# Kernel tuning notes

Hardware: AMD Instinct MI355X
Metric: run time of the kernel (lower is better)

## Reference

```python
import jax, jax.numpy as jnp
import numpy as np

C = 256      # in/out channels
PSI = 4
W = C // PSI          # window width = 64
D = W // 2            # stride = 32
HEADS = 2 * PSI - 1   # 7


def conv_bn_relu(x, Wmat, scale, bias):
    # 1x1 conv (no bias) + inference-mode BN (folded to per-channel scale/bias) + ReLU
    y = jnp.einsum('oc,bcn->bon', Wmat, x)
    return jax.nn.relu(y * scale[:, None] + bias[:, None])


def setup_inputs() -> dict:
    key = jax.random.key(0)
    ks = jax.random.split(key, 16)
    B, N = 4, 2048
    x = jax.random.normal(ks[0], (B, C, N), dtype=jnp.float32)
    Wq = jax.random.normal(ks[1], (C, C), dtype=jnp.float32) / np.sqrt(C)
    Wk = jax.random.normal(ks[2], (C, C), dtype=jnp.float32) / np.sqrt(C)
    Wv = jax.random.normal(ks[3], (C, C), dtype=jnp.float32) / np.sqrt(C)
    sq = jax.random.uniform(ks[4], (C,), dtype=jnp.float32, minval=0.5, maxval=1.5)
    bq = jax.random.normal(ks[5], (C,), dtype=jnp.float32) * 0.1
    sk = jax.random.uniform(ks[6], (C,), dtype=jnp.float32, minval=0.5, maxval=1.5)
    bk = jax.random.normal(ks[7], (C,), dtype=jnp.float32) * 0.1
    sv = jax.random.uniform(ks[8], (C,), dtype=jnp.float32, minval=0.5, maxval=1.5)
    bv = jax.random.normal(ks[9], (C,), dtype=jnp.float32) * 0.1
    Wf = jax.random.normal(ks[10], (C, HEADS * W), dtype=jnp.float32) / np.sqrt(HEADS * W)
    bf = jax.random.normal(ks[11], (C,), dtype=jnp.float32) * 0.1
    sf = jax.random.uniform(ks[12], (C,), dtype=jnp.float32, minval=0.5, maxval=1.5)
    bff = jax.random.normal(ks[13], (C,), dtype=jnp.float32) * 0.1
    return dict(x=x, Wq=Wq, sq=sq, bq=bq, Wk=Wk, sk=sk, bk=bk,
                Wv=Wv, sv=sv, bv=bv, Wf=Wf, bf=bf, sf=sf, bff=bff)


def reference(x, Wq, sq, bq, Wk, sk, bk, Wv, sv, bv, Wf, bf, sf, bff):
    q = conv_bn_relu(x, Wq, sq, bq)   # [B, C, N]
    k = conv_bn_relu(x, Wk, sk, bk)
    v = conv_bn_relu(x, Wv, sv, bv)

    # overlapping channel windows: head m covers channels [m*D, m*D+W)
    win = jnp.arange(HEADS)[:, None] * D + jnp.arange(W)[None, :]  # [HEADS, W]
    qw = q[:, win, :]  # [B, HEADS, W, N]
    kw = k[:, win, :]
    vw = v[:, win, :]

    # a_m = q_m^T k_m over channel window -> [B, HEADS, N, N]
    attn = jnp.einsum('bhwn,bhwm->bhnm', qw, kw)
    attn = jax.nn.softmax(attn, axis=-1)
    # o_m = (a_m v_m^T)^T -> [B, HEADS, W, N]
    o = jnp.einsum('bhnm,bhwm->bhwn', attn, vw)

    B, _, _, N = o.shape
    O = o.reshape(B, HEADS * W, N)  # concat heads along channel dim

    # fusion: 1x1 conv (with bias) + BN + ReLU
    y = jnp.einsum('oc,bcn->bon', Wf, O) + bf[:, None]
    return jax.nn.relu(y * sf[:, None] + bff[:, None])
```

## Files before the change

### kernel.cpp

```cpp
#include <hip/hip_runtime.h>
#include <hip/hip_bf16.h>

typedef __attribute__((ext_vector_type(8))) short bf16x8;
typedef __attribute__((ext_vector_type(4))) float f32x4;

namespace {
constexpr int kC = 256;
constexpr int kN = 2048;
constexpr int kB = 4;
constexpr int kHeads = 7;
constexpr int kOC = kHeads * 64;
constexpr int kSplit = 2;
constexpr int kMChunk = kN / kSplit;
constexpr float kLog2e = 1.44269504f;
}

static __device__ __forceinline__ float bf2f(ushort u) {
    union { unsigned u; float f; } v; v.u = ((unsigned)u) << 16;
    return v.f;
}
static __device__ __forceinline__ unsigned pk_bf16(float a, float b) {
    __hip_bfloat162 h = __float22bfloat162_rn(make_float2(a, b));
    union { __hip_bfloat162 h; unsigned u; } v; v.h = h;
    return v.u;
}
static __device__ __forceinline__ ushort4 pack4bf(float a, float b, float c, float d) {
    union { ushort4 s; uint2 u; } v;
    v.u.x = pk_bf16(a, b); v.u.y = pk_bf16(c, d);
    return v.s;
}
static __device__ __forceinline__ float fexp2(float x) {
#if __has_builtin(__builtin_amdgcn_exp2f)
    return __builtin_amdgcn_exp2f(x);
#else
    return exp2f(x);
#endif
}
static __device__ __forceinline__ void g2l16(const ushort* g, ushort* l) {
    __builtin_amdgcn_global_load_lds(
        (const __attribute__((address_space(1))) void*)g,
        (__attribute__((address_space(3))) void*)l,
        16, 0, 0);
}

__global__ __launch_bounds__(256) void cast_w_kernel(
    const float* __restrict__ Wq, const float* __restrict__ Wk,
    const float* __restrict__ Wv, const float* __restrict__ Wf,
    ushort* __restrict__ wq, ushort* __restrict__ wk,
    ushort* __restrict__ wv, ushort* __restrict__ wf)
{
    int which = blockIdx.y;
    const float* src = which == 0 ? Wq : which == 1 ? Wk : which == 2 ? Wv : Wf;
    ushort* dst      = which == 0 ? wq : which == 1 ? wk : which == 2 ? wv : wf;
    int n = (which == 3) ? kC * kOC : kC * kC;
    int i = (blockIdx.x * 256 + threadIdx.x) * 4;
    if (i < n) {
        float4 v = *(const float4*)(src + i);
        *(ushort4*)(dst + i) = pack4bf(v.x, v.y, v.z, v.w);
    }
}

__global__ __launch_bounds__(256) void transpose_kernel(
    const float* __restrict__ x, ushort* __restrict__ xT)
{
    const int nt = blockIdx.x, ct = blockIdx.y, b = blockIdx.z;
    __shared__ float T[64][65];
    const int tid = threadIdx.x;
    const float* xb = x + ((size_t)b * kC + ct * 64) * kN + nt * 64;
#pragma unroll
    for (int p = 0; p < 16; ++p) {
        int idx = p * 256 + tid;
        int cc = idx >> 6, nn = idx & 63;
        T[cc][nn] = xb[(size_t)cc * kN + nn];
    }
    __syncthreads();
    ushort* xTb = xT + ((size_t)b * kN + nt * 64) * kC + ct * 64;
#pragma unroll
    for (int p = 0; p < 4; ++p) {
        int nn = p * 16 + (tid >> 4);
        int c4 = (tid & 15) * 4;
        *(ushort4*)&xTb[(size_t)nn * kC + c4] =
            pack4bf(T[c4 + 0][nn], T[c4 + 1][nn], T[c4 + 2][nn], T[c4 + 3][nn]);
    }
}

__global__ __launch_bounds__(256, 2) void qkv_kernel(
    const ushort* __restrict__ xT,
    const ushort* __restrict__ Wqb, const ushort* __restrict__ Wkb, const ushort* __restrict__ Wvb,
    const float* __restrict__ sq, const float* __restrict__ bq,
    const float* __restrict__ sk, const float* __restrict__ bk,
    const float* __restrict__ sv, const float* __restrict__ bv,
    ushort* __restrict__ qT, ushort* __restrict__ kT, ushort* __restrict__ vB)
{
    const int nt  = blockIdx.x;
    const int ot  = blockIdx.y;
    const int b   = blockIdx.z / 3;
    const int mat = blockIdx.z % 3;
    const ushort* Wb = mat == 0 ? Wqb : mat == 1 ? Wkb : Wvb;
    const float* sm = mat == 0 ? sq : mat == 1 ? sk : sv;
    const float* bm = mat == 0 ? bq : mat == 1 ? bk : bv;

    __shared__ __align__(16) ushort lds[4][128 * 64];

    const int tid = threadIdx.x;
    const int lane = tid & 63, wav = tid >> 6;
    const int quad = lane >> 4, l16 = lane & 15;

    const ushort* xTb = xT + ((size_t)b * kN + nt * 128) * kC;
    const ushort* Wt  = Wb + (size_t)(ot * 128) * kC;

    f32x4 acc[8][2];
#pragma unroll
    for (int mt = 0; mt < 8; ++mt)
#pragma unroll
        for (int ntt = 0; ntt < 2; ++ntt)
#pragma unroll
            for (int r = 0; r < 4; ++r) acc[mt][ntt][r] = 0.f;

    const int sa   = lane >> 3;
    const int sblk = (lane & 7) ^ sa;
    auto dmaK = [&](int k0, int buf) {
#pragma unroll
        for (int p = 0; p < 4; ++p) {
            int row = wav * 32 + p * 8 + sa;
            size_t so = (size_t)row * kC + k0 + sblk * 8;
            int dbase = (wav * 32 + p * 8) * 64;
            g2l16(Wt + so,  &lds[buf][dbase]);
            g2l16(xTb + so, &lds[2 + buf][dbase]);
        }
    };

    dmaK(0, 0);
    __syncthreads();

    for (int kt = 0; kt < 4; ++kt) {
        const int cur = kt & 1;
        const bool more = (kt < 3);
        if (more) dmaK((kt + 1) * 64, cur ^ 1);

        const ushort* rowB = (mat < 2) ? lds[cur] : lds[2 + cur];
        const ushort* colB = (mat < 2) ? lds[2 + cur] : lds[cur];
#pragma unroll
        for (int ks = 0; ks < 2; ++ks) {
            bf16x8 bfr[2];
#pragma unroll
            for (int ntt = 0; ntt < 2; ++ntt) {
                int row = wav * 32 + ntt * 16 + l16;
                bfr[ntt] = *(const bf16x8*)&colB[row * 64 + (((ks * 4 + quad) ^ (row & 7)) * 8)];
            }
#pragma unroll
            for (int mt = 0; mt < 8; ++mt) {
                int row = mt * 16 + l16;
                bf16x8 af = *(const bf16x8*)&rowB[row * 64 + (((ks * 4 + quad) ^ (row & 7)) * 8)];
#pragma unroll
                for (int ntt = 0; ntt < 2; ++ntt)
                    acc[mt][ntt] = __builtin_amdgcn_mfma_f32_16x16x32_bf16(
                        af, bfr[ntt], acc[mt][ntt], 0, 0, 0);
            }
        }
        __syncthreads();
    }

    ushort* sT = &lds[0][0];
    const float qs = (mat == 0) ? kLog2e : 1.f;

    if (mat < 2) {
#pragma unroll
        for (int mt = 0; mt < 8; ++mt) {
            float4 sc4 = *(const float4*)&sm[ot * 128 + mt * 16 + quad * 4];
            float4 bi4 = *(const float4*)&bm[ot * 128 + mt * 16 + quad * 4];
#pragma unroll
            for (int ntt = 0; ntt < 2; ++ntt) {
                int nrow = wav * 32 + ntt * 16 + l16;
                float v0 = fmaf(acc[mt][ntt][0], sc4.x, bi4.x) * qs;
                float v1 = fmaf(acc[mt][ntt][1], sc4.y, bi4.y) * qs;
                float v2 = fmaf(acc[mt][ntt][2], sc4.z, bi4.z) * qs;
                float v3 = fmaf(acc[mt][ntt][3], sc4.w, bi4.w) * qs;
                int cb = (mt * 2 + (quad >> 1)) ^ (nrow & 15);
                *(ushort4*)&sT[nrow * 128 + cb * 8 + (quad & 1) * 4] =
                    pack4bf(v0 > 0.f ? v0 : 0.f, v1 > 0.f ? v1 : 0.f,
                            v2 > 0.f ? v2 : 0.f, v3 > 0.f ? v3 : 0.f);
            }
        }
        __syncthreads();
        ushort* out = (mat == 0) ? qT : kT;
#pragma unroll
        for (int p = 0; p < 8; ++p) {
            int idx = p * 256 + tid;
            int row = idx >> 4, blk = idx & 15;
            int4 d = *(const int4*)&sT[row * 128 + ((blk ^ (row & 15)) * 8)];
            *(int4*)&out[((size_t)b * kN + nt * 128 + row) * kC + ot * 128 + blk * 8] = d;
        }
    } else {
#pragma unroll
        for (int ntt = 0; ntt < 2; ++ntt) {
            int orow = wav * 32 + ntt * 16 + l16;
            float sc = sm[ot * 128 + orow], bi = bm[ot * 128 + orow];
#pragma unroll
            for (int mt = 0; mt < 8; ++mt) {
                float v0 = fmaf(acc[mt][ntt][0], sc, bi);
                float v1 = fmaf(acc[mt][ntt][1], sc, bi);
                float v2 = fmaf(acc[mt][ntt][2], sc, bi);
                float v3 = fmaf(acc[mt][ntt][3], sc, bi);
                int cb = (mt * 2 + (quad >> 1)) ^ (orow & 15);
                *(ushort4*)&sT[orow * 128 + cb * 8 + (quad & 1) * 4] =
                    pack4bf(v0 > 0.f ? v0 : 0.f, v1 > 0.f ? v1 : 0.f,
                            v2 > 0.f ? v2 : 0.f, v3 > 0.f ? v3 : 0.f);
            }
        }
        __syncthreads();
#pragma unroll
        for (int p = 0; p < 8; ++p) {
            int idx = p * 256 + tid;
            int row = idx >> 4, blk = idx & 15;
            int4 d = *(const int4*)&sT[row * 128 + ((blk ^ (row & 15)) * 8)];
            *(int4*)&vB[((size_t)b * kC + ot * 128 + row) * kN + nt * 128 + blk * 8] = d;
        }
    }
}

__global__ __launch_bounds__(512, 4) void attn_kernel(
    const ushort* __restrict__ qT, const ushort* __restrict__ kT,
    const ushort* __restrict__ vB,
    ushort* __restrict__ Opart, float* __restrict__ Ls)
{
    const int j   = blockIdx.x;
    const int lid = (j & 7) * 56 + (j >> 3);
    const int nt  = lid & 7;
    const int rest = lid >> 3;
    const int h = rest % 7;
    const int z = rest / 7;
    const int s = z & 1;
    const int b = z >> 1;
    const int n0 = nt * 256;

    const int tid = threadIdx.x;
    const int lane = tid & 63, wav = tid >> 6;
    const int quad = lane >> 4, l16 = lane & 15;

    __shared__ __align__(16) ushort sKV[2][8192];

    const ushort* qTb = qT + (size_t)b * kN * kC;
    const ushort* kTb = kT + (size_t)b * kN * kC;
    const ushort* vbb = vB + ((size_t)b * kC + h * 32) * kN;

    const int arr   = wav >> 2;
    const int rbase = (wav & 3) * 16;

    bf16x8 qf[2][2];
#pragma unroll
    for (int kk = 0; kk < 2; ++kk)
#pragma unroll
        for (int nt2 = 0; nt2 < 2; ++nt2) {
            int ng = n0 + wav * 32 + nt2 * 16 + l16;
            qf[kk][nt2] = *(const bf16x8*)(qTb + (size_t)ng * kC + h * 32 + kk * 32 + quad * 8);
        }

    f32x4 oacc[4][2];
#pragma unroll
    for (int wt = 0; wt < 4; ++wt)
#pragma unroll
        for (int nt2 = 0; nt2 < 2; ++nt2)
#pragma unroll
            for (int r = 0; r < 4; ++r) oacc[wt][nt2][r] = 0.f;
    float li[2] = {0.f, 0.f};

    const int mstart = s * kMChunk;
    const int NIT = kMChunk / 64;

    const int sa   = lane >> 3;
    const int sblk = (lane & 7) ^ sa;
    auto dmaTile = [&](int m0, int buf) {
#pragma unroll
        for (int p = 0; p < 2; ++p) {
            int rl = rbase + p * 8 + sa;
            const ushort* src = (arr == 0)
                ? (kTb + (size_t)(m0 + rl) * kC + h * 32 + sblk * 8)
                : (vbb + (size_t)rl * kN + m0 + sblk * 8);
            g2l16(src, &sKV[buf][arr * 4096 + (rbase + p * 8) * 64]);
        }
    };

    dmaTile(mstart, 0);
    __syncthreads();

    for (int it = 0; it < NIT; ++it) {
        const int cur = it & 1;
        const bool more = (it + 1 < NIT);
        if (more) dmaTile(mstart + (it + 1) * 64, cur ^ 1);

        const ushort* sK = &sKV[cur][0];
        const ushort* sV = &sKV[cur][4096];

        f32x4 sacc[4][2];
#pragma unroll
        for (int mt = 0; mt < 4; ++mt)
#pragma unroll
            for (int nt2 = 0; nt2 < 2; ++nt2)
#pragma unroll
                for (int r = 0; r < 4; ++r) sacc[mt][nt2][r] = 0.f;
        __builtin_amdgcn_s_setprio(1);
#pragma unroll
        for (int kk = 0; kk < 2; ++kk)
#pragma unroll
            for (int mt = 0; mt < 4; ++mt) {
                int row = mt * 16 + l16;
                bf16x8 af = *(const bf16x8*)&sK[row * 64 + (((kk * 4 + quad) ^ (row & 7)) * 8)];
#pragma unroll
                for (int nt2 = 0; nt2 < 2; ++nt2)
                    sacc[mt][nt2] = __builtin_amdgcn_mfma_f32_16x16x32_bf16(
                        af, qf[kk][nt2], sacc[mt][nt2], 0, 0, 0);
            }
        __builtin_amdgcn_s_setprio(0);

        unsigned d[2][4][2];
#pragma unroll
        for (int nt2 = 0; nt2 < 2; ++nt2) {
            float sum = 0.f;
#pragma unroll
            for (int mt = 0; mt < 4; ++mt) {
                float p0 = fexp2(sacc[mt][nt2][0]);
                float p1 = fexp2(sacc[mt][nt2][1]);
                float p2 = fexp2(sacc[mt][nt2][2]);
                float p3 = fexp2(sacc[mt][nt2][3]);
                sum += (p0 + p1) + (p2 + p3);
                d[nt2][mt][0] = pk_bf16(p0, p1);
                d[nt2][mt][1] = pk_bf16(p2, p3);
            }
            sum += __shfl_xor(sum, 16);
            sum += __shfl_xor(sum, 32);
            li[nt2] += sum;
        }

#pragma unroll
        for (int ks = 0; ks < 2; ++ks) {
            bf16x8 pf[2];
#pragma unroll
            for (int nt2 = 0; nt2 < 2; ++nt2) {
                union { unsigned w[4]; bf16x8 v8; } pu;
#if __has_builtin(__builtin_amdgcn_permlane32_swap) && __has_builtin(__builtin_amdgcn_permlane16_swap)
#pragma unroll
                for (int rd = 0; rd < 2; ++rd) {
                    unsigned a = d[nt2][2 * ks][rd], bb = d[nt2][2 * ks + 1][rd];
                    auto r32 = __builtin_amdgcn_permlane32_swap(a, bb, false, false);
                    auto r16 = __builtin_amdgcn_permlane16_swap(r32[0], r32[1], false, false);
                    pu.w[rd]     = r16[0];
                    pu.w[2 + rd] = r16[1];
                }
#else
                const int gx = ((lane & 16) << 1) + l16;
                const int gy = gx + 16;
                const bool lo = (lane < 32);
#pragma unroll
                for (int rd = 0; rd < 2; ++rd) {
                    unsigned u = d[nt2][2 * ks][rd], v = d[nt2][2 * ks + 1][rd];
                    unsigned xu = (unsigned)__shfl((int)u, gx);
                    unsigned xv = (unsigned)__shfl((int)v, gx);
                    unsigned yu = (unsigned)__shfl((int)u, gy);
                    unsigned yv = (unsigned)__shfl((int)v, gy);
                    pu.w[rd]     = lo ? xu : xv;
                    pu.w[2 + rd] = lo ? yu : yv;
                }
#endif
                pf[nt2] = pu.v8;
            }
            __builtin_amdgcn_s_setprio(1);
#pragma unroll
            for (int wt = 0; wt < 4; ++wt) {
                int wr = wt * 16 + l16;
                bf16x8 vf = *(const bf16x8*)&sV[wr * 64 + (((ks * 4 + quad) ^ (wr & 7)) * 8)];
#pragma unroll
                for (int nt2 = 0; nt2 < 2; ++nt2)
                    oacc[wt][nt2] = __builtin_amdgcn_mfma_f32_16x16x32_bf16(
                        vf, pf[nt2], oacc[wt][nt2], 0, 0, 0);
            }
            __builtin_amdgcn_s_setprio(0);
        }

        __syncthreads();
    }

#pragma unroll
    for (int nt2 = 0; nt2 < 2; ++nt2) {
        if (quad == 0) {
            int n = n0 + wav * 32 + nt2 * 16 + l16;
            size_t si = ((size_t)(s * kB + b) * kHeads + h) * kN + n;
            Ls[si] = li[nt2];
        }
    }
    ushort* sT = &sKV[0][0];
#pragma unroll
    for (int wt = 0; wt < 4; ++wt)
#pragma unroll
        for (int nt2 = 0; nt2 < 2; ++nt2) {
            float inv = 1.f / li[nt2];
            int nrow = wav * 32 + nt2 * 16 + l16;
            int cb = (wt * 2 + (quad >> 1)) ^ (nrow & 7);
            *(ushort4*)&sT[nrow * 64 + cb * 8 + (quad & 1) * 4] =
                pack4bf(oacc[wt][nt2][0] * inv, oacc[wt][nt2][1] * inv,
                        oacc[wt][nt2][2] * inv, oacc[wt][nt2][3] * inv);
        }
    __syncthreads();
    int rsub = tid >> 3, blk = tid & 7;
#pragma unroll
    for (int p = 0; p < 4; ++p) {
        int row = p * 64 + rsub;
        int4 dd = *(const int4*)&sT[row * 64 + ((blk ^ (row & 7)) * 8)];
        *(int4*)&Opart[((size_t)s * kB * kN + (size_t)b * kN + n0 + row) * kOC
                       + h * 64 + blk * 8] = dd;
    }
}

__global__ __launch_bounds__(256, 4) void proj_kernel(
    const ushort* __restrict__ Opart, const float* __restrict__ Ls,
    const ushort* __restrict__ Wfb,
    const float* __restrict__ bf_, const float* __restrict__ sf,
    const float* __restrict__ bff, float* __restrict__ out)
{
    const int nt = blockIdx.x;
    const int ot = blockIdx.y;
    const int b  = blockIdx.z;
    __shared__ __align__(16) ushort sA[2][64 * 64];
    __shared__ __align__(16) ushort sB[2][64 * 64];
    const int tid = threadIdx.x;
    const int lane = tid & 63, wav = tid >> 6;
    const int quad = lane >> 4, l16 = lane & 15;

    const ushort* Wt  = Wfb + (size_t)(ot * 64) * kOC;
    const ushort* Op1 = Opart;
    const ushort* Op2 = Opart + (size_t)kB * kN * kOC;
    const size_t soff = (size_t)kB * kHeads * kN;

    f32x4 acc[4];
#pragma unroll
    for (int ntt = 0; ntt < 4; ++ntt)
#pragma unroll
        for (int r = 0; r < 4; ++r) acc[ntt][r] = 0.f;

    int4 areg[2], b1reg[2], b2reg[2];
    float w1a[2], w2a[2];

    auto prefetch = [&](int kt) {
        int k0 = kt * 64;
#pragma unroll
        for (int p = 0; p < 2; ++p) {
            int idx = p * 256 + tid, row = idx >> 3, blk = idx & 7;
            areg[p] = *(const int4*)(Wt + (size_t)row * kOC + k0 + blk * 8);
            int n = nt * 64 + row;
            size_t bo = ((size_t)b * kN + n) * kOC + k0 + blk * 8;
            b1reg[p] = *(const int4*)(Op1 + bo);
            b2reg[p] = *(const int4*)(Op2 + bo);
            size_t si = ((size_t)b * kHeads + kt) * kN + n;
            float l1 = Ls[si], l2 = Ls[si + soff];
            float inv = 1.f / (l1 + l2);
            w1a[p] = l1 * inv; w2a[p] = l2 * inv;
        }
    };
    auto stage = [&](int buf) {
#pragma unroll
        for (int p = 0; p < 2; ++p) {
            int idx = p * 256 + tid, row = idx >> 3, blk = idx & 7;
            *(int4*)&sA[buf][row * 64 + ((blk ^ (row & 7)) * 8)] = areg[p];
            union { int4 v; ushort u[8]; } a, c;
            a.v = b1reg[p]; c.v = b2reg[p];
            float rr[8];
#pragma unroll
            for (int j = 0; j < 8; ++j)
                rr[j] = bf2f(a.u[j]) * w1a[p] + bf2f(c.u[j]) * w2a[p];
            int4 o;
            o.x = (int)pk_bf16(rr[0], rr[1]);
            o.y = (int)pk_bf16(rr[2], rr[3]);
            o.z = (int)pk_bf16(rr[4], rr[5]);
            o.w = (int)pk_bf16(rr[6], rr[7]);
            *(int4*)&sB[buf][row * 64 + ((blk ^ (row & 7)) * 8)] = o;
        }
    };

    prefetch(0);
    stage(0);
    __syncthreads();

    for (int kt = 0; kt < 7; ++kt) {
        const int cur = kt & 1;
        const bool more = (kt < 6);
        if (more) prefetch(kt + 1);
#pragma unroll
        for (int ks = 0; ks < 2; ++ks) {
            int arow = wav * 16 + l16;
            bf16x8 af = *(const bf16x8*)&sA[cur][arow * 64 + (((ks * 4 + quad) ^ (arow & 7)) * 8)];
#pragma unroll
            for (int ntt = 0; ntt < 4; ++ntt) {
                int brow = ntt * 16 + l16;
                bf16x8 bfr = *(const bf16x8*)&sB[cur][brow * 64 + (((ks * 4 + quad) ^ (brow & 7)) * 8)];
                acc[ntt] = __builtin_amdgcn_mfma_f32_16x16x32_bf16(af, bfr, acc[ntt], 0, 0, 0);
            }
        }
        if (more) stage(cur ^ 1);
        __syncthreads();
    }
#pragma unroll
    for (int r = 0; r < 4; ++r) {
        int o = ot * 64 + wav * 16 + quad * 4 + r;
        float bfv = bf_[o], sfv = sf[o], bffv = bff[o];
#pragma unroll
        for (int ntt = 0; ntt < 4; ++ntt) {
            int n = nt * 64 + ntt * 16 + l16;
            float y = fmaf(acc[ntt][r] + bfv, sfv, bffv);
            out[((size_t)b * kC + o) * kN + n] = y > 0.f ? y : 0.f;
        }
    }
}

extern "C" void kernel_launch(void* const* d_in, const int* in_sizes, int n_in,
                              void* d_out, int out_size, void* d_ws, size_t ws_size,
                              hipStream_t stream) {
    const float* x   = (const float*)d_in[0];
    const float* Wq  = (const float*)d_in[1];
    const float* sq  = (const float*)d_in[2];
    const float* bq  = (const float*)d_in[3];
    const float* Wk  = (const float*)d_in[4];
    const float* sk  = (const float*)d_in[5];
    const float* bk  = (const float*)d_in[6];
    const float* Wv  = (const float*)d_in[7];
    const float* sv  = (const float*)d_in[8];
    const float* bv  = (const float*)d_in[9];
    const float* Wf  = (const float*)d_in[10];
    const float* bf_ = (const float*)d_in[11];
    const float* sf  = (const float*)d_in[12];
    const float* bff = (const float*)d_in[13];
    float* out = (float*)d_out;

    char* ws = (char*)d_ws;
    ushort* xT  = (ushort*)(ws);
    ushort* Wqb = (ushort*)(ws + 4194304);
    ushort* Wkb = (ushort*)(ws + 4325376);
    ushort* Wvb = (ushort*)(ws + 4456448);
    ushort* Wfb = (ushort*)(ws + 4587520);
    ushort* qT  = (ushort*)(ws + 4816896);
    ushort* kT  = (ushort*)(ws + 9011200);
    ushort* vB  = (ushort*)(ws + 13205504);
    ushort* Opart = (ushort*)(ws + 17399808);
    float*  Ls  = (float*)(ws + 32079872);

    cast_w_kernel<<<dim3(112, 4), 256, 0, stream>>>(Wq, Wk, Wv, Wf, Wqb, Wkb, Wvb, Wfb);
    transpose_kernel<<<dim3(kN / 64, kC / 64, kB), 256, 0, stream>>>(x, xT);
    qkv_kernel<<<dim3(kN / 128, kC / 128, kB * 3), 256, 0, stream>>>(
        xT, Wqb, Wkb, Wvb, sq, bq, sk, bk, sv, bv, qT, kT, vB);
    attn_kernel<<<dim3(448), 512, 0, stream>>>(
        qT, kT, vB, Opart, Ls);
    proj_kernel<<<dim3(kN / 64, kC / 64, kB), 256, 0, stream>>>(
        Opart, Ls, Wfb, bf_, sf, bff, out);
}
```

Measured before the change: 156.7 us.

## Merge prep kernels, widen QKV blocks to 512 threads, relax attn occupancy

Merges the weight-cast and input-transpose kernels into one launch, with blocks branching on block index, to save a launch. The QKV GEMM moves to 512-thread blocks that split the 128x128 tile across 8 waves, halving per-wave accumulators, and uses a swizzled 1D grid for XCD locality. The attention kernel's launch bounds drop from 4 to 2 blocks per SM, giving the compiler more registers at the cost of occupancy.

```diff
diff --git a/kernel.cpp b/kernel.cpp
--- a/kernel.cpp
+++ b/kernel.cpp
@@ -43,48 +43,50 @@
         16, 0, 0);
 }
 
-__global__ __launch_bounds__(256) void cast_w_kernel(
+__global__ __launch_bounds__(256) void prep_kernel(
+    const float* __restrict__ x,
     const float* __restrict__ Wq, const float* __restrict__ Wk,
     const float* __restrict__ Wv, const float* __restrict__ Wf,
+    ushort* __restrict__ xT,
     ushort* __restrict__ wq, ushort* __restrict__ wk,
     ushort* __restrict__ wv, ushort* __restrict__ wf)
 {
-    int which = blockIdx.y;
-    const float* src = which == 0 ? Wq : which == 1 ? Wk : which == 2 ? Wv : Wf;
-    ushort* dst      = which == 0 ? wq : which == 1 ? wk : which == 2 ? wv : wf;
-    int n = (which == 3) ? kC * kOC : kC * kC;
-    int i = (blockIdx.x * 256 + threadIdx.x) * 4;
-    if (i < n) {
-        float4 v = *(const float4*)(src + i);
-        *(ushort4*)(dst + i) = pack4bf(v.x, v.y, v.z, v.w);
-    }
-}
-
-__global__ __launch_bounds__(256) void transpose_kernel(
-    const float* __restrict__ x, ushort* __restrict__ xT)
-{
-    const int nt = blockIdx.x, ct = blockIdx.y, b = blockIdx.z;
     __shared__ float T[64][65];
+    const int bid = blockIdx.x;
     const int tid = threadIdx.x;
-    const float* xb = x + ((size_t)b * kC + ct * 64) * kN + nt * 64;
-#pragma unroll
-    for (int p = 0; p < 16; ++p) {
-        int idx = p * 256 + tid;
-        int cc = idx >> 6, nn = idx & 63;
-        T[cc][nn] = xb[(size_t)cc * kN + nn];
-    }
-    __syncthreads();
-    ushort* xTb = xT + ((size_t)b * kN + nt * 64) * kC + ct * 64;
-#pragma unroll
-    for (int p = 0; p < 4; ++p) {
-        int nn = p * 16 + (tid >> 4);
-        int c4 = (tid & 15) * 4;
-        *(ushort4*)&xTb[(size_t)nn * kC + c4] =
-            pack4bf(T[c4 + 0][nn], T[c4 + 1][nn], T[c4 + 2][nn], T[c4 + 3][nn]);
-    }
-}
-
-__global__ __launch_bounds__(256, 2) void qkv_kernel(
+    if (bid < 512) {
+        const int nt = bid & 31, ct = (bid >> 5) & 3, b = bid >> 7;
+        const float* xb = x + ((size_t)b * kC + ct * 64) * kN + nt * 64;
+#pragma unroll
+        for (int p = 0; p < 16; ++p) {
+            int idx = p * 256 + tid;
+            int cc = idx >> 6, nn = idx & 63;
+            T[cc][nn] = xb[(size_t)cc * kN + nn];
+        }
+        __syncthreads();
+        ushort* xTb = xT + ((size_t)b * kN + nt * 64) * kC + ct * 64;
+#pragma unroll
+        for (int p = 0; p < 4; ++p) {
+            int nn = p * 16 + (tid >> 4);
+            int c4 = (tid & 15) * 4;
+            *(ushort4*)&xTb[(size_t)nn * kC + c4] =
+                pack4bf(T[c4 + 0][nn], T[c4 + 1][nn], T[c4 + 2][nn], T[c4 + 3][nn]);
+        }
+    } else {
+        const int j = bid - 512;
+        const int which = j / 112, bx = j % 112;
+        const float* src = which == 0 ? Wq : which == 1 ? Wk : which == 2 ? Wv : Wf;
+        ushort* dst      = which == 0 ? wq : which == 1 ? wk : which == 2 ? wv : wf;
+        int n = (which == 3) ? kC * kOC : kC * kC;
+        int i = (bx * 256 + tid) * 4;
+        if (i < n) {
+            float4 v = *(const float4*)(src + i);
+            *(ushort4*)(dst + i) = pack4bf(v.x, v.y, v.z, v.w);
+        }
+    }
+}
+
+__global__ __launch_bounds__(512, 2) void qkv_kernel(
     const ushort* __restrict__ xT,
     const ushort* __restrict__ Wqb, const ushort* __restrict__ Wkb, const ushort* __restrict__ Wvb,
     const float* __restrict__ sq, const float* __restrict__ bq,
@@ -92,10 +94,13 @@
     const float* __restrict__ sv, const float* __restrict__ bv,
     ushort* __restrict__ qT, ushort* __restrict__ kT, ushort* __restrict__ vB)
 {
-    const int nt  = blockIdx.x;
-    const int ot  = blockIdx.y;
-    const int b   = blockIdx.z / 3;
-    const int mat = blockIdx.z % 3;
+    const int j   = blockIdx.x;
+    const int lid = (j & 7) * 48 + (j >> 3);
+    const int nt  = lid & 15;
+    const int ot  = (lid >> 4) & 1;
+    const int zz  = lid >> 5;
+    const int b   = zz / 3;
+    const int mat = zz % 3;
     const ushort* Wb = mat == 0 ? Wqb : mat == 1 ? Wkb : Wvb;
     const float* sm = mat == 0 ? sq : mat == 1 ? sk : sv;
     const float* bm = mat == 0 ? bq : mat == 1 ? bk : bv;
@@ -105,13 +110,15 @@
     const int tid = threadIdx.x;
     const int lane = tid & 63, wav = tid >> 6;
     const int quad = lane >> 4, l16 = lane & 15;
+    const int oh = wav >> 2;
+    const int nq = wav & 3;
 
     const ushort* xTb = xT + ((size_t)b * kN + nt * 128) * kC;
     const ushort* Wt  = Wb + (size_t)(ot * 128) * kC;
 
-    f32x4 acc[8][2];
-#pragma unroll
-    for (int mt = 0; mt < 8; ++mt)
+    f32x4 acc[4][2];
+#pragma unroll
+    for (int mt = 0; mt < 4; ++mt)
 #pragma unroll
         for (int ntt = 0; ntt < 2; ++ntt)
 #pragma unroll
@@ -121,10 +128,10 @@
     const int sblk = (lane & 7) ^ sa;
     auto dmaK = [&](int k0, int buf) {
 #pragma unroll
-        for (int p = 0; p < 4; ++p) {
-            int row = wav * 32 + p * 8 + sa;
+        for (int p = 0; p < 2; ++p) {
+            int row = wav * 16 + p * 8 + sa;
             size_t so = (size_t)row * kC + k0 + sblk * 8;
-            int dbase = (wav * 32 + p * 8) * 64;
+            int dbase = (wav * 16 + p * 8) * 64;
             g2l16(Wt + so,  &lds[buf][dbase]);
             g2l16(xTb + so, &lds[2 + buf][dbase]);
         }
@@ -145,12 +152,12 @@
             bf16x8 bfr[2];
 #pragma unroll
             for (int ntt = 0; ntt < 2; ++ntt) {
-                int row = wav * 32 + ntt * 16 + l16;
+                int row = nq * 32 + ntt * 16 + l16;
                 bfr[ntt] = *(const bf16x8*)&colB[row * 64 + (((ks * 4 + quad) ^ (row & 7)) * 8)];
             }
 #pragma unroll
-            for (int mt = 0; mt < 8; ++mt) {
-                int row = mt * 16 + l16;
+            for (int mt = 0; mt < 4; ++mt) {
+                int row = oh * 64 + mt * 16 + l16;
                 bf16x8 af = *(const bf16x8*)&rowB[row * 64 + (((ks * 4 + quad) ^ (row & 7)) * 8)];
 #pragma unroll
                 for (int ntt = 0; ntt < 2; ++ntt)
@@ -166,17 +173,17 @@
 
     if (mat < 2) {
 #pragma unroll
-        for (int mt = 0; mt < 8; ++mt) {
-            float4 sc4 = *(const float4*)&sm[ot * 128 + mt * 16 + quad * 4];
-            float4 bi4 = *(const float4*)&bm[ot * 128 + mt * 16 + quad * 4];
+        for (int mt = 0; mt < 4; ++mt) {
+            float4 sc4 = *(const float4*)&sm[ot * 128 + oh * 64 + mt * 16 + quad * 4];
+            float4 bi4 = *(const float4*)&bm[ot * 128 + oh * 64 + mt * 16 + quad * 4];
 #pragma unroll
             for (int ntt = 0; ntt < 2; ++ntt) {
-                int nrow = wav * 32 + ntt * 16 + l16;
+                int nrow = nq * 32 + ntt * 16 + l16;
                 float v0 = fmaf(acc[mt][ntt][0], sc4.x, bi4.x) * qs;
                 float v1 = fmaf(acc[mt][ntt][1], sc4.y, bi4.y) * qs;
                 float v2 = fmaf(acc[mt][ntt][2], sc4.z, bi4.z) * qs;
                 float v3 = fmaf(acc[mt][ntt][3], sc4.w, bi4.w) * qs;
-                int cb = (mt * 2 + (quad >> 1)) ^ (nrow & 15);
+                int cb = (oh * 8 + mt * 2 + (quad >> 1)) ^ (nrow & 15);
                 *(ushort4*)&sT[nrow * 128 + cb * 8 + (quad & 1) * 4] =
                     pack4bf(v0 > 0.f ? v0 : 0.f, v1 > 0.f ? v1 : 0.f,
                             v2 > 0.f ? v2 : 0.f, v3 > 0.f ? v3 : 0.f);
@@ -185,8 +192,8 @@
         __syncthreads();
         ushort* out = (mat == 0) ? qT : kT;
 #pragma unroll
-        for (int p = 0; p < 8; ++p) {
-            int idx = p * 256 + tid;
+        for (int p = 0; p < 4; ++p) {
+            int idx = p * 512 + tid;
             int row = idx >> 4, blk = idx & 15;
             int4 d = *(const int4*)&sT[row * 128 + ((blk ^ (row & 15)) * 8)];
             *(int4*)&out[((size_t)b * kN + nt * 128 + row) * kC + ot * 128 + blk * 8] = d;
@@ -194,15 +201,15 @@
     } else {
 #pragma unroll
         for (int ntt = 0; ntt < 2; ++ntt) {
-            int orow = wav * 32 + ntt * 16 + l16;
+            int orow = nq * 32 + ntt * 16 + l16;
             float sc = sm[ot * 128 + orow], bi = bm[ot * 128 + orow];
 #pragma unroll
-            for (int mt = 0; mt < 8; ++mt) {
+            for (int mt = 0; mt < 4; ++mt) {
                 float v0 = fmaf(acc[mt][ntt][0], sc, bi);
                 float v1 = fmaf(acc[mt][ntt][1], sc, bi);
                 float v2 = fmaf(acc[mt][ntt][2], sc, bi);
                 float v3 = fmaf(acc[mt][ntt][3], sc, bi);
-                int cb = (mt * 2 + (quad >> 1)) ^ (orow & 15);
+                int cb = (oh * 8 + mt * 2 + (quad >> 1)) ^ (orow & 15);
                 *(ushort4*)&sT[orow * 128 + cb * 8 + (quad & 1) * 4] =
                     pack4bf(v0 > 0.f ? v0 : 0.f, v1 > 0.f ? v1 : 0.f,
                             v2 > 0.f ? v2 : 0.f, v3 > 0.f ? v3 : 0.f);
@@ -210,8 +217,8 @@
         }
         __syncthreads();
 #pragma unroll
-        for (int p = 0; p < 8; ++p) {
-            int idx = p * 256 + tid;
+        for (int p = 0; p < 4; ++p) {
+            int idx = p * 512 + tid;
             int row = idx >> 4, blk = idx & 15;
             int4 d = *(const int4*)&sT[row * 128 + ((blk ^ (row & 15)) * 8)];
             *(int4*)&vB[((size_t)b * kC + ot * 128 + row) * kN + nt * 128 + blk * 8] = d;
@@ -219,7 +226,7 @@
     }
 }
 
-__global__ __launch_bounds__(512, 4) void attn_kernel(
+__global__ __launch_bounds__(512, 2) void attn_kernel(
     const ushort* __restrict__ qT, const ushort* __restrict__ kT,
     const ushort* __restrict__ vB,
     ushort* __restrict__ Opart, float* __restrict__ Ls)
@@ -465,8 +472,8 @@
             a.v = b1reg[p]; c.v = b2reg[p];
             float rr[8];
 #pragma unroll
-            for (int j = 0; j < 8; ++j)
-                rr[j] = bf2f(a.u[j]) * w1a[p] + bf2f(c.u[j]) * w2a[p];
+            for (int jj = 0; jj < 8; ++jj)
+                rr[jj] = bf2f(a.u[jj]) * w1a[p] + bf2f(c.u[jj]) * w2a[p];
             int4 o;
             o.x = (int)pk_bf16(rr[0], rr[1]);
             o.y = (int)pk_bf16(rr[2], rr[3]);
@@ -542,9 +549,9 @@
     ushort* Opart = (ushort*)(ws + 17399808);
     float*  Ls  = (float*)(ws + 32079872);
 
-    cast_w_kernel<<<dim3(112, 4), 256, 0, stream>>>(Wq, Wk, Wv, Wf, Wqb, Wkb, Wvb, Wfb);
-    transpose_kernel<<<dim3(kN / 64, kC / 64, kB), 256, 0, stream>>>(x, xT);
-    qkv_kernel<<<dim3(kN / 128, kC / 128, kB * 3), 256, 0, stream>>>(
+    prep_kernel<<<dim3(960), 256, 0, stream>>>(
+        x, Wq, Wk, Wv, Wf, xT, Wqb, Wkb, Wvb, Wfb);
+    qkv_kernel<<<dim3(384), 512, 0, stream>>>(
         xT, Wqb, Wkb, Wvb, sq, bq, sk, bk, sv, bv, qT, kT, vB);
     attn_kernel<<<dim3(448), 512, 0, stream>>>(
         qT, kT, vB, Opart, Ls);
```

New measurement: 153.6 us. About the same (-1.9%).
